# Kernel tuning notes

Measured on AMD Instinct MI355X. Metric: run time of the kernel, lower is better.

## Reference

```python
import jax, jax.numpy as jnp
import numpy as np

N, D, R, O = 4096, 128, 256, 64


def setup_inputs() -> dict:
    key = jax.random.key(0)
    k1, k2, k3, k4 = jax.random.split(key, 4)
    X = jax.random.normal(k1, (N, D), dtype=jnp.float32)
    # Gaussian membership params per rule: centers and (positive) widths, shape [R, D]
    centers = 0.5 * jax.random.normal(k2, (R, D), dtype=jnp.float32)
    sigmas = 1.5 + jax.random.uniform(k3, (R, D), dtype=jnp.float32)  # in [1.5, 2.5]
    # Takagi-Sugeno per-rule linear coeffs [R, D+1, O] (last row = bias)
    coeffs = 0.02 * jax.random.normal(k4, (R, D + 1, O), dtype=jnp.float32)
    return {"X": X, "centers": centers, "sigmas": sigmas, "coeffs": coeffs}


def reference(X, centers, sigmas, coeffs):
    # Layer 1: Gaussian memberships for all rules at once: [N, R, D]
    diff = X[:, None, :] - centers[None, :, :]
    memb = jnp.exp(-(diff * diff) / (2.0 * sigmas * sigmas)[None, :, :])
    # Layer 2: rule strengths via product over input dims ('prod' strategy): [N, R]
    strengths = jnp.prod(memb, axis=2)
    # Layer 3: normalize across rules
    norm = strengths / (jnp.sum(strengths, axis=1, keepdims=True) + 1e-8)
    # Layer 4: per-rule linear consequents: [N, R, O]
    weighted = jnp.einsum('ni,rij->nrj', X, coeffs[:, :-1, :]) + coeffs[:, -1, :][None, :, :]
    # Layer 5: weighted combine over rules: [N, O]
    out = jnp.einsum('nr,nrj->nj', norm, weighted)
    # task='classification' -> Softmax(dim=1)
    return jax.nn.softmax(out, axis=1)
```

## Files before the change

kernel.cpp:

```cpp
#include <hip/hip_runtime.h>

#define N_SAMPLES 4096
#define D_IN      128
#define R_RULES   256
#define O_OUT     64
#define KPAD      136
#define NCHUNK    17
#define CH_I      8
#define NGROUPS   8

typedef _Float16 f16;
typedef _Float16 f16x2 __attribute__((ext_vector_type(2)));
typedef _Float16 f16x4 __attribute__((ext_vector_type(4)));
typedef _Float16 f16x8 __attribute__((ext_vector_type(8)));
typedef float    f32x4 __attribute__((ext_vector_type(4)));

__global__ __launch_bounds__(256) void anfis_prep_all(
    const float* __restrict__ coeffs, const float* __restrict__ centers,
    const float* __restrict__ sigmas, f16* __restrict__ Cp,
    f16* __restrict__ Bext) {
  __shared__ alignas(16) f16 T[64 * 32];
  __shared__ float red[4];
  const int bid = blockIdx.x;
  const int tid = threadIdx.x;

  if (bid < 1088) {
    const int g = bid / 136;
    const int i = bid - g * 136;
    const int rg = tid & 31;
    const int jb = tid >> 5;
    if (i < 129) {
      const float* src = coeffs + ((size_t)(g * 32 + rg) * 129 + i) * 64 + jb * 8;
      float4 a = reinterpret_cast<const float4*>(src)[0];
      float4 b = reinterpret_cast<const float4*>(src)[1];
      T[(jb * 8 + 0) * 32 + rg] = (f16)a.x;
      T[(jb * 8 + 1) * 32 + rg] = (f16)a.y;
      T[(jb * 8 + 2) * 32 + rg] = (f16)a.z;
      T[(jb * 8 + 3) * 32 + rg] = (f16)a.w;
      T[(jb * 8 + 4) * 32 + rg] = (f16)b.x;
      T[(jb * 8 + 5) * 32 + rg] = (f16)b.y;
      T[(jb * 8 + 6) * 32 + rg] = (f16)b.z;
      T[(jb * 8 + 7) * 32 + rg] = (f16)b.w;
    } else {
#pragma unroll
      for (int q = 0; q < 8; ++q) T[(jb * 8 + q) * 32 + rg] = (f16)0.0f;
    }
    __syncthreads();
    f16x8* dst = reinterpret_cast<f16x8*>(Cp + ((size_t)g * KPAD + i) * 2048);
    const int j = tid >> 2, blk = tid & 3;
    dst[(j << 2) | (blk ^ ((j >> 1) & 3))] = reinterpret_cast<const f16x8*>(T)[tid];
  } else {
    const int sub = tid >> 7;
    const int d = tid & 127;
    const int r = ((bid - 1088) << 1) + sub;
    const float c = centers[(size_t)r * 128 + d];
    const float s = sigmas[(size_t)r * 128 + d];
    const float iv = 0.5f / (s * s);
    const float b1 = -iv;
    const float b2 = 2.0f * c * iv;
    f16 b1h = (f16)b1; f16 b1l = (f16)(b1 - (float)b1h);
    f16 b2h = (f16)b2; f16 b2l = (f16)(b2 - (float)b2h);
    auto put = [&](int k, f16 v) {
      Bext[((size_t)(k >> 3) * 256 + r) * 8 + (k & 7)] = v;
    };
    put(d, b1h);
    put(128 + d, b1l);
    put(256 + d, b1h);
    put(384 + d, b2h);
    put(512 + d, b2l);
    put(640 + d, b2h);
    float p = -c * c * iv;
#pragma unroll
    for (int off = 32; off; off >>= 1) p += __shfl_xor(p, off, 64);
    if ((tid & 63) == 0) red[tid >> 6] = p;
    __syncthreads();
    if (d < 30) put(770 + d, (f16)0.0f);
    if (d == 0) {
      float k2 = red[sub * 2] + red[sub * 2 + 1];
      f16 h = (f16)k2; f16 l = (f16)(k2 - (float)h);
      put(768, h);
      put(769, l);
    }
  }
}

__global__ __launch_bounds__(512) void anfis_s16n(
    const float* __restrict__ X, const f16* __restrict__ Bext,
    f16* __restrict__ P) {
  __shared__ alignas(16) f16 Xq[16 * 512];
  __shared__ float rowsum[16][8];
  const int tid = threadIdx.x;
  const int m0 = blockIdx.x * 16;
  const int w = tid >> 6, lane = tid & 63;
  const int lm = lane & 15, quad = lane >> 4;

  if (tid < 256) {
    int m = tid >> 4, oct = tid & 15;
    const float* src = X + (size_t)(m0 + m) * 128 + oct * 8;
    float4 a = reinterpret_cast<const float4*>(src)[0];
    float4 b = reinterpret_cast<const float4*>(src)[1];
    float xs[8] = {a.x, a.y, a.z, a.w, b.x, b.y, b.z, b.w};
    f16x8 vh, vl, v2h, v2l;
#pragma unroll
    for (int q = 0; q < 8; ++q) {
      float x = xs[q];
      f16 h = (f16)x;   f16 l = (f16)(x - (float)h);
      float x2 = x * x;
      f16 h2 = (f16)x2; f16 l2 = (f16)(x2 - (float)h2);
      vh[q] = h; vl[q] = l; v2h[q] = h2; v2l[q] = l2;
    }
    f16x8* row = reinterpret_cast<f16x8*>(&Xq[m * 512]);
    int sw = m & 7;
    row[(0 * 16 + oct) ^ sw] = v2h;
    row[(1 * 16 + oct) ^ sw] = v2l;
    row[(2 * 16 + oct) ^ sw] = vh;
    row[(3 * 16 + oct) ^ sw] = vl;
  }
  __syncthreads();

  f32x4 acc[2] = {};
  const f16x8* arow = reinterpret_cast<const f16x8*>(&Xq[lm * 512]);
  const int asw = lm & 7;
  const int col0 = w * 32 + lm;

#pragma unroll
  for (int t = 0; t < 24; ++t) {
    const int seg = t >> 2;
    const int plane = (seg < 2) ? 0 : (seg == 2) ? 1 : (seg < 5) ? 2 : 3;
    const int o = t * 4 + quad;
    f16x8 av = arow[(plane * 16 + (o & 15)) ^ asw];
    const f16* bp = Bext + ((size_t)o * 256 + col0) * 8;
    f16x8 b0 = *reinterpret_cast<const f16x8*>(bp);
    f16x8 b1 = *reinterpret_cast<const f16x8*>(bp + 16 * 8);
    acc[0] = __builtin_amdgcn_mfma_f32_16x16x32_f16(av, b0, acc[0], 0, 0, 0);
    acc[1] = __builtin_amdgcn_mfma_f32_16x16x32_f16(av, b1, acc[1], 0, 0, 0);
  }
  {
    f16x8 av = {};
    if (quad == 0) { av[0] = (f16)1.0f; av[1] = (f16)1.0f; }
    const int o = 96 + quad;
    const f16* bp = Bext + ((size_t)o * 256 + col0) * 8;
    f16x8 b0 = *reinterpret_cast<const f16x8*>(bp);
    f16x8 b1 = *reinterpret_cast<const f16x8*>(bp + 16 * 8);
    acc[0] = __builtin_amdgcn_mfma_f32_16x16x32_f16(av, b0, acc[0], 0, 0, 0);
    acc[1] = __builtin_amdgcn_mfma_f32_16x16x32_f16(av, b1, acc[1], 0, 0, 0);
  }

  float e[2][4];
#pragma unroll
  for (int nf = 0; nf < 2; ++nf)
#pragma unroll
    for (int q = 0; q < 4; ++q) e[nf][q] = __expf(acc[nf][q]);

  float rp[4];
#pragma unroll
  for (int q = 0; q < 4; ++q) {
    rp[q] = e[0][q] + e[1][q];
#pragma unroll
    for (int msk = 1; msk < 16; msk <<= 1) rp[q] += __shfl_xor(rp[q], msk, 64);
  }
  if (lm == 0)
#pragma unroll
    for (int q = 0; q < 4; ++q) rowsum[quad * 4 + q][w] = rp[q];
  __syncthreads();

#pragma unroll
  for (int q = 0; q < 4; ++q) {
    const int row = quad * 4 + q;
    float s8 = 0.f;
#pragma unroll
    for (int w2 = 0; w2 < 8; ++w2) s8 += rowsum[row][w2];
    const float inv = 1.0f / (s8 + 1e-8f);
#pragma unroll
    for (int nf = 0; nf < 2; ++nf)
      P[(size_t)(m0 + row) * R_RULES + w * 32 + nf * 16 + lm] =
          (f16)(e[nf][q] * inv);
  }
}

__global__ __launch_bounds__(256) void anfis_main16(
    const float* __restrict__ X, const f16* __restrict__ P,
    const f16* __restrict__ Cp, float* __restrict__ part) {
  __shared__ alignas(16) f16 Xs[64 * KPAD];
  __shared__ alignas(16) f16 Bs[CH_I * 64 * 32];
  const int tid = threadIdx.x;
  const int g = blockIdx.x & 7;
  const int m0 = (blockIdx.x >> 3) * 64;
  const int w = tid >> 6, lane = tid & 63;
  const int mg = w >> 1, ng = w & 1;
  const int lm = lane & 15, quad = lane >> 4;

#pragma unroll
  for (int it = 0; it < 8; ++it) {
    int fi = tid + (it << 8);
    int m = fi >> 5, k4 = (fi & 31) << 2;
    float4 v = reinterpret_cast<const float4*>(X)[(size_t)(m0 + m) * 32 + (fi & 31)];
    f16x4 h = {(f16)v.x, (f16)v.y, (f16)v.z, (f16)v.w};
    *reinterpret_cast<f16x4*>(&Xs[m * KPAD + k4]) = h;
  }
  if (tid < 64) {
    f16x8 bias = {};
    bias[0] = (f16)1.0f;
    *reinterpret_cast<f16x8*>(&Xs[tid * KPAD + 128]) = bias;
  }

  union F8 { f16x8 v; f16x2 h[4]; };
  F8 pf[2];
#pragma unroll
  for (int mf = 0; mf < 2; ++mf) {
    int row = m0 + mg * 32 + mf * 16 + lm;
    pf[mf].v = *reinterpret_cast<const f16x8*>(
        &P[(size_t)row * R_RULES + g * 32 + quad * 8]);
  }

  f32x4 acc[2][2] = {};
  const char* cpg = (const char*)Cp + (size_t)g * KPAD * 4096;
  const int bswz = (quad ^ ((lm >> 1) & 3)) * 8;

  for (int c = 0; c < NCHUNK; ++c) {
    __syncthreads();
    const char* gsrc = cpg + (size_t)c * 32768;
#pragma unroll
    for (int it = 0; it < 8; ++it) {
      int off = (it << 12) + (w << 10);
      __builtin_amdgcn_global_load_lds(
          (const __attribute__((address_space(1))) unsigned int*)(gsrc + off + lane * 16),
          (__attribute__((address_space(3))) unsigned int*)((char*)Bs + off),
          16, 0, 0);
    }
    __syncthreads();
    f16x8 xv[2];
    xv[0] = *reinterpret_cast<const f16x8*>(&Xs[(mg * 32 + lm) * KPAD + c * 8]);
    xv[1] = *reinterpret_cast<const f16x8*>(&Xs[(mg * 32 + 16 + lm) * KPAD + c * 8]);
#pragma unroll
    for (int ii = 0; ii < CH_I; ++ii) {
      F8 a[2];
#pragma unroll
      for (int mf = 0; mf < 2; ++mf) {
        f16 xvv = xv[mf][ii];
        f16x2 xd = {xvv, xvv};
        a[mf].h[0] = pf[mf].h[0] * xd;
        a[mf].h[1] = pf[mf].h[1] * xd;
        a[mf].h[2] = pf[mf].h[2] * xd;
        a[mf].h[3] = pf[mf].h[3] * xd;
      }
      const f16* brow = &Bs[(ii * 64 + ng * 32 + lm) * 32 + bswz];
      f16x8 b0 = *reinterpret_cast<const f16x8*>(brow);
      f16x8 b1 = *reinterpret_cast<const f16x8*>(brow + 16 * 32);
      acc[0][0] = __builtin_amdgcn_mfma_f32_16x16x32_f16(a[0].v, b0, acc[0][0], 0, 0, 0);
      acc[0][1] = __builtin_amdgcn_mfma_f32_16x16x32_f16(a[0].v, b1, acc[0][1], 0, 0, 0);
      acc[1][0] = __builtin_amdgcn_mfma_f32_16x16x32_f16(a[1].v, b0, acc[1][0], 0, 0, 0);
      acc[1][1] = __builtin_amdgcn_mfma_f32_16x16x32_f16(a[1].v, b1, acc[1][1], 0, 0, 0);
    }
  }

#pragma unroll
  for (int mf = 0; mf < 2; ++mf)
#pragma unroll
    for (int nf = 0; nf < 2; ++nf)
#pragma unroll
      for (int q = 0; q < 4; ++q) {
        int row = m0 + mg * 32 + mf * 16 + quad * 4 + q;
        int col = ng * 32 + nf * 16 + lm;
        part[((size_t)g * N_SAMPLES + row) * O_OUT + col] = acc[mf][nf][q];
      }
}

__global__ __launch_bounds__(256) void anfis_out(
    const float* __restrict__ part, float* __restrict__ out) {
  const int n = blockIdx.x * 4 + (threadIdx.x >> 6);
  const int lane = threadIdx.x & 63;
  const size_t stride = (size_t)N_SAMPLES * O_OUT;
  const float* p0 = part + (size_t)n * O_OUT + lane;
  float v = 0.f;
#pragma unroll
  for (int gg = 0; gg < 8; ++gg) v += p0[gg * stride];
  float mx = v;
#pragma unroll
  for (int off = 32; off; off >>= 1) mx = fmaxf(mx, __shfl_xor(mx, off, 64));
  float e = __expf(v - mx);
  float s = e;
#pragma unroll
  for (int off = 32; off; off >>= 1) s += __shfl_xor(s, off, 64);
  out[(size_t)n * O_OUT + lane] = e / s;
}

extern "C" void kernel_launch(void* const* d_in, const int* in_sizes, int n_in,
                              void* d_out, int out_size, void* d_ws, size_t ws_size,
                              hipStream_t stream) {
  const float* X       = (const float*)d_in[0];
  const float* centers = (const float*)d_in[1];
  const float* sigmas  = (const float*)d_in[2];
  const float* coeffs  = (const float*)d_in[3];
  float* out = (float*)d_out;

  float* part = (float*)d_ws;
  f16*   Cp   = (f16*)(part + (size_t)NGROUPS * N_SAMPLES * O_OUT);
  f16*   Bext = Cp + (size_t)NGROUPS * KPAD * 2048;
  f16*   P    = Bext + (size_t)100 * 256 * 8;

  anfis_prep_all<<<1088 + 128, 256, 0, stream>>>(coeffs, centers, sigmas, Cp, Bext);
  anfis_s16n<<<N_SAMPLES / 16, 512, 0, stream>>>(X, Bext, P);
  anfis_main16<<<512, 256, 0, stream>>>(X, P, Cp, part);
  anfis_out<<<N_SAMPLES / 4, 256, 0, stream>>>(part, out);
}
```

Baseline: 103.0 us.

## Split K in two and widen M tile to 128 rows per block in main kernel

The main GEMM kernel now gives each block 128 rows and half of the K dimension (input features plus bias), with every wave covering all 64 outputs. Each loaded B tile is therefore reused by more rows. The number of partial-sum planes doubles to 16, which the output kernel sums. The intent is to cut the Cp tile traffic per row and to raise occupancy with smaller LDS chunks and launch bounds. In exchange the partial buffer and its reduction traffic double.

```diff
diff --git a/kernel.cpp b/kernel.cpp
--- a/kernel.cpp
+++ b/kernel.cpp
@@ -5,9 +5,11 @@
 #define R_RULES   256
 #define O_OUT     64
 #define KPAD      136
-#define NCHUNK    17
-#define CH_I      8
+#define KHALF     68
+#define CH        4
+#define NCH       17
 #define NGROUPS   8
+#define NPLANES   16
 
 typedef _Float16 f16;
 typedef _Float16 f16x2 __attribute__((ext_vector_type(2)));
@@ -178,50 +180,58 @@
   }
 }
 
-__global__ __launch_bounds__(256) void anfis_main16(
+__global__ __launch_bounds__(256, 4) void anfis_main16(
     const float* __restrict__ X, const f16* __restrict__ P,
     const f16* __restrict__ Cp, float* __restrict__ part) {
-  __shared__ alignas(16) f16 Xs[64 * KPAD];
-  __shared__ alignas(16) f16 Bs[CH_I * 64 * 32];
+  __shared__ alignas(16) f16 Xs[128 * 72];
+  __shared__ alignas(16) f16 Bs[CH * 64 * 32];
   const int tid = threadIdx.x;
   const int g = blockIdx.x & 7;
-  const int m0 = (blockIdx.x >> 3) * 64;
+  const int ks = (blockIdx.x >> 3) & 1;
+  const int m0 = (blockIdx.x >> 4) * 128;
   const int w = tid >> 6, lane = tid & 63;
-  const int mg = w >> 1, ng = w & 1;
   const int lm = lane & 15, quad = lane >> 4;
 
-#pragma unroll
-  for (int it = 0; it < 8; ++it) {
-    int fi = tid + (it << 8);
-    int m = fi >> 5, k4 = (fi & 31) << 2;
-    float4 v = reinterpret_cast<const float4*>(X)[(size_t)(m0 + m) * 32 + (fi & 31)];
-    f16x4 h = {(f16)v.x, (f16)v.y, (f16)v.z, (f16)v.w};
-    *reinterpret_cast<f16x4*>(&Xs[m * KPAD + k4]) = h;
-  }
-  if (tid < 64) {
-    f16x8 bias = {};
-    bias[0] = (f16)1.0f;
-    *reinterpret_cast<f16x8*>(&Xs[tid * KPAD + 128]) = bias;
+  {
+    const int m = tid >> 1;
+    const int cbase = (tid & 1) * 9;
+#pragma unroll
+    for (int it = 0; it < 9; ++it) {
+      const int col = cbase + it;
+      const int gi = ks * KHALF + col * 4;
+      f16x4 h;
+      if (gi + 3 < 128) {
+        float4 v = *reinterpret_cast<const float4*>(
+            X + (size_t)(m0 + m) * 128 + gi);
+        h = f16x4{(f16)v.x, (f16)v.y, (f16)v.z, (f16)v.w};
+      } else if (gi == 128) {
+        h = f16x4{(f16)1.0f, (f16)0.0f, (f16)0.0f, (f16)0.0f};
+      } else {
+        h = f16x4{};
+      }
+      *reinterpret_cast<f16x4*>(&Xs[m * 72 + col * 4]) = h;
+    }
   }
 
   union F8 { f16x8 v; f16x2 h[4]; };
   F8 pf[2];
 #pragma unroll
   for (int mf = 0; mf < 2; ++mf) {
-    int row = m0 + mg * 32 + mf * 16 + lm;
+    int row = m0 + w * 32 + mf * 16 + lm;
     pf[mf].v = *reinterpret_cast<const f16x8*>(
         &P[(size_t)row * R_RULES + g * 32 + quad * 8]);
   }
 
-  f32x4 acc[2][2] = {};
-  const char* cpg = (const char*)Cp + (size_t)g * KPAD * 4096;
+  f32x4 acc[2][4] = {};
+  const char* cpg = (const char*)Cp + (size_t)g * KPAD * 4096
+                  + (size_t)ks * KHALF * 4096;
   const int bswz = (quad ^ ((lm >> 1) & 3)) * 8;
 
-  for (int c = 0; c < NCHUNK; ++c) {
+  for (int c = 0; c < NCH; ++c) {
     __syncthreads();
-    const char* gsrc = cpg + (size_t)c * 32768;
-#pragma unroll
-    for (int it = 0; it < 8; ++it) {
+    const char* gsrc = cpg + (size_t)c * 16384;
+#pragma unroll
+    for (int it = 0; it < 4; ++it) {
       int off = (it << 12) + (w << 10);
       __builtin_amdgcn_global_load_lds(
           (const __attribute__((address_space(1))) unsigned int*)(gsrc + off + lane * 16),
@@ -229,11 +239,11 @@
           16, 0, 0);
     }
     __syncthreads();
-    f16x8 xv[2];
-    xv[0] = *reinterpret_cast<const f16x8*>(&Xs[(mg * 32 + lm) * KPAD + c * 8]);
-    xv[1] = *reinterpret_cast<const f16x8*>(&Xs[(mg * 32 + 16 + lm) * KPAD + c * 8]);
-#pragma unroll
-    for (int ii = 0; ii < CH_I; ++ii) {
+    f16x4 xv[2];
+    xv[0] = *reinterpret_cast<const f16x4*>(&Xs[(w * 32 + lm) * 72 + c * 4]);
+    xv[1] = *reinterpret_cast<const f16x4*>(&Xs[(w * 32 + 16 + lm) * 72 + c * 4]);
+#pragma unroll
+    for (int ii = 0; ii < CH; ++ii) {
       F8 a[2];
 #pragma unroll
       for (int mf = 0; mf < 2; ++mf) {
@@ -244,25 +254,26 @@
         a[mf].h[2] = pf[mf].h[2] * xd;
         a[mf].h[3] = pf[mf].h[3] * xd;
       }
-      const f16* brow = &Bs[(ii * 64 + ng * 32 + lm) * 32 + bswz];
-      f16x8 b0 = *reinterpret_cast<const f16x8*>(brow);
-      f16x8 b1 = *reinterpret_cast<const f16x8*>(brow + 16 * 32);
-      acc[0][0] = __builtin_amdgcn_mfma_f32_16x16x32_f16(a[0].v, b0, acc[0][0], 0, 0, 0);
-      acc[0][1] = __builtin_amdgcn_mfma_f32_16x16x32_f16(a[0].v, b1, acc[0][1], 0, 0, 0);
-      acc[1][0] = __builtin_amdgcn_mfma_f32_16x16x32_f16(a[1].v, b0, acc[1][0], 0, 0, 0);
-      acc[1][1] = __builtin_amdgcn_mfma_f32_16x16x32_f16(a[1].v, b1, acc[1][1], 0, 0, 0);
-    }
-  }
-
+#pragma unroll
+      for (int nf = 0; nf < 4; ++nf) {
+        f16x8 b = *reinterpret_cast<const f16x8*>(
+            &Bs[(ii * 64 + nf * 16 + lm) * 32 + bswz]);
+        acc[0][nf] = __builtin_amdgcn_mfma_f32_16x16x32_f16(a[0].v, b, acc[0][nf], 0, 0, 0);
+        acc[1][nf] = __builtin_amdgcn_mfma_f32_16x16x32_f16(a[1].v, b, acc[1][nf], 0, 0, 0);
+      }
+    }
+  }
+
+  const int plane = ks * 8 + g;
 #pragma unroll
   for (int mf = 0; mf < 2; ++mf)
 #pragma unroll
-    for (int nf = 0; nf < 2; ++nf)
+    for (int nf = 0; nf < 4; ++nf)
 #pragma unroll
       for (int q = 0; q < 4; ++q) {
-        int row = m0 + mg * 32 + mf * 16 + quad * 4 + q;
-        int col = ng * 32 + nf * 16 + lm;
-        part[((size_t)g * N_SAMPLES + row) * O_OUT + col] = acc[mf][nf][q];
+        int row = m0 + w * 32 + mf * 16 + quad * 4 + q;
+        int col = nf * 16 + lm;
+        part[((size_t)plane * N_SAMPLES + row) * O_OUT + col] = acc[mf][nf][q];
       }
 }
 
@@ -274,7 +285,7 @@
   const float* p0 = part + (size_t)n * O_OUT + lane;
   float v = 0.f;
 #pragma unroll
-  for (int gg = 0; gg < 8; ++gg) v += p0[gg * stride];
+  for (int gg = 0; gg < NPLANES; ++gg) v += p0[gg * stride];
   float mx = v;
 #pragma unroll
   for (int off = 32; off; off >>= 1) mx = fmaxf(mx, __shfl_xor(mx, off, 64));
@@ -295,7 +306,7 @@
   float* out = (float*)d_out;
 
   float* part = (float*)d_ws;
-  f16*   Cp   = (f16*)(part + (size_t)NGROUPS * N_SAMPLES * O_OUT);
+  f16*   Cp   = (f16*)(part + (size_t)NPLANES * N_SAMPLES * O_OUT);
   f16*   Bext = Cp + (size_t)NGROUPS * KPAD * 2048;
   f16*   P    = Bext + (size_t)100 * 256 * 8;
 
```

After: 105.3 us. 1.02x slower.
